# Kernel optimization log

Measured on AMD Instinct MI355X. Metric: run time of the kernel, lower is better.

## Reference

```python
import jax, jax.numpy as jnp
import numpy as np

P_FACTOR = 3.0
EPS = 1e-12  # torch F.normalize eps


def _l2norm(x):
    # F.normalize(x, dim=1): divide by max(||x||_2, eps) along feature dim
    n = jnp.sqrt(jnp.sum(x * x, axis=1, keepdims=True))
    return x / jnp.maximum(n, EPS)


def setup_inputs() -> dict:
    key = jax.random.key(0)
    ks = jax.random.split(key, 7)
    B, N, F, E = 4096, 20000, 768, 512
    X = jax.random.normal(ks[0], (B, F), jnp.float32)
    D = jax.random.normal(ks[1], (N, F), jnp.float32)
    r = jax.random.uniform(ks[2], (N, 1), jnp.float32)  # correctness in [0,1]
    g_w = jax.random.normal(ks[3], (E, F), jnp.float32) * (1.0 / np.sqrt(F))
    g_b = jax.random.normal(ks[4], (E,), jnp.float32) * 0.01
    h_w = jax.random.normal(ks[5], (1, 1), jnp.float32)
    h_b = jax.random.normal(ks[6], (1,), jnp.float32) * 0.01
    return {"X": X, "D": D, "r": r, "g_w": g_w, "g_b": g_b, "h_w": h_w, "h_b": h_b}


def reference(X, D, r, g_w, g_b, h_w, h_b):
    # register_buffer path: r = ex_correct * 2 - 1
    r = r * 2.0 - 1.0
    # g: Linear(feat_dim -> feat_embed_dim) on both queries and exemplars
    Xe = X @ g_w.T + g_b            # [B, E]
    De = D @ g_w.T + g_b            # [N, E]
    # h: Linear(1 -> class_embed_dim)
    rh = r @ h_w.T + h_b            # [N, C]
    # Minerva: cosine similarity -> power-law activation -> weighted retrieval
    a = _l2norm(Xe) @ _l2norm(De).T                 # [B, N]
    a = jnp.sign(a) * jnp.abs(a) ** P_FACTOR        # |s|^p * sign(s)
    logits = a @ rh                                 # [B, C]
    preds = jax.nn.sigmoid(logits)
    return logits, preds
```

## Files before the change

kernel.cpp:

```cpp
#include <hip/hip_runtime.h>
#include <cstdint>


typedef __attribute__((ext_vector_type(4))) float  f32x4;
typedef __attribute__((ext_vector_type(8))) __bf16 bf16x8;
typedef __attribute__((ext_vector_type(4))) __bf16 bf16x4;

constexpr int B = 4096, N = 20000, F = 768, E = 512;

#define AS1CAST(p) ((__attribute__((address_space(1))) unsigned int*)(uintptr_t)(p))
#define AS3CAST(p) ((__attribute__((address_space(3))) unsigned int*)(uintptr_t)(p))

__device__ __forceinline__ void gload_lds16(const void* g, void* l) {
  __builtin_amdgcn_global_load_lds(AS1CAST(g), AS3CAST(l), 16, 0, 0);
}


__global__ void k_prep(const float* __restrict__ X, const float* __restrict__ D,
                       const float* __restrict__ G, const float* __restrict__ r,
                       const float* __restrict__ hw, const float* __restrict__ hb,
                       __bf16* __restrict__ Xb, __bf16* __restrict__ Db,
                       __bf16* __restrict__ Gb, float* __restrict__ rh,
                       float* __restrict__ lg, float* __restrict__ norm2) {
  const int t = blockIdx.x * blockDim.x + threadIdx.x;
  const int stride = gridDim.x * blockDim.x;
  constexpr int nX = B * F / 4, nD = N * F / 4, nG = E * F / 4;
  constexpr int tot = nX + nD + nG;
  for (int i = t; i < tot; i += stride) {
    const float4* src; bf16x4* dst; int off;
    if (i < nX)           { src = (const float4*)X; dst = (bf16x4*)Xb; off = i; }
    else if (i < nX + nD) { src = (const float4*)D; dst = (bf16x4*)Db; off = i - nX; }
    else                  { src = (const float4*)G; dst = (bf16x4*)Gb; off = i - nX - nD; }
    float4 v = src[off];
    bf16x4 o;
    o[0] = (__bf16)v.x; o[1] = (__bf16)v.y; o[2] = (__bf16)v.z; o[3] = (__bf16)v.w;
    dst[off] = o;
  }
  if (t < N) rh[t] = (2.0f * r[t] - 1.0f) * hw[0] + hb[0];
  if (t < B) lg[t] = 0.0f;
  if (t < B + N) norm2[t] = 0.0f;
}


__global__ __launch_bounds__(256, 2)
void k_embed(const __bf16* __restrict__ Xb, const __bf16* __restrict__ Db,
             const __bf16* __restrict__ Gb, const float* __restrict__ bias,
             __bf16* __restrict__ Eb, float* __restrict__ norm2) {
  constexpr int K = F;
  __shared__ __bf16 As[128 * 32];
  __shared__ __bf16 Bs[128 * 32];
  __shared__ float ssum[128];
  const int tid  = threadIdx.x;
  const int wave = tid >> 6;
  const int lane = tid & 63;
  const int by = blockIdx.y;
  const bool isX = (by < B / 128);
  const __bf16* A = isX ? Xb : Db;
  const int m0 = isX ? by * 128 : (by - B / 128) * 128;
  const int Mr = isX ? B : N;
  const int g0 = by * 128;
  const int n0 = blockIdx.x * 128;
  if (tid < 128) ssum[tid] = 0.0f;

  const int r_in = lane >> 2;
  const int kp   = (lane & 3) * 8;
  int ar0 = m0 + wave * 16 + r_in;        if (ar0 >= Mr) ar0 = Mr - 1;
  int ar1 = m0 + (wave + 4) * 16 + r_in;  if (ar1 >= Mr) ar1 = Mr - 1;
  const int br0 = n0 + wave * 16 + r_in;
  const int br1 = n0 + (wave + 4) * 16 + r_in;

  const __bf16* ga0 = A + (size_t)ar0 * K + kp;
  const __bf16* ga1 = A + (size_t)ar1 * K + kp;
  const __bf16* gb0 = Gb + (size_t)br0 * K + kp;
  const __bf16* gb1 = Gb + (size_t)br1 * K + kp;
  __bf16* la0 = &As[(size_t)wave * 512 + (size_t)lane * 8];
  __bf16* la1 = &As[(size_t)(wave + 4) * 512 + (size_t)lane * 8];
  __bf16* lb0 = &Bs[(size_t)wave * 512 + (size_t)lane * 8];
  __bf16* lb1 = &Bs[(size_t)(wave + 4) * 512 + (size_t)lane * 8];

  const int mw = (wave & 1) * 64;
  const int nw = (wave >> 1) * 64;
  const int quad = lane >> 4;
  const int l15  = lane & 15;

  f32x4 acc[4][4] = {};

  for (int kb = 0; kb < K; kb += 32) {
    gload_lds16(ga0 + kb, la0);
    gload_lds16(ga1 + kb, la1);
    gload_lds16(gb0 + kb, lb0);
    gload_lds16(gb1 + kb, lb1);
    __syncthreads();
    bf16x8 af[4], bfr[4];
#pragma unroll
    for (int i = 0; i < 4; ++i)
      af[i] = *(const bf16x8*)&As[(mw + i * 16 + l15) * 32 + quad * 8];
#pragma unroll
    for (int j = 0; j < 4; ++j)
      bfr[j] = *(const bf16x8*)&Bs[(nw + j * 16 + l15) * 32 + quad * 8];
#pragma unroll
    for (int i = 0; i < 4; ++i)
#pragma unroll
      for (int j = 0; j < 4; ++j)
        acc[i][j] = __builtin_amdgcn_mfma_f32_16x16x32_bf16(af[i], bfr[j], acc[i][j], 0, 0, 0);
    __syncthreads();
  }

#pragma unroll
  for (int i = 0; i < 4; ++i) {
    float part[4] = {0.0f, 0.0f, 0.0f, 0.0f};
#pragma unroll
    for (int j = 0; j < 4; ++j) {
      const int col = n0 + nw + j * 16 + l15;
      const float bv = bias[col];
#pragma unroll
      for (int rr = 0; rr < 4; ++rr) {
        const int row = mw + i * 16 + quad * 4 + rr;
        if (m0 + row < Mr) {
          const __bf16 hv = (__bf16)(acc[i][j][rr] + bv);
          Eb[(size_t)(g0 + row) * E + col] = hv;
          const float vb = (float)hv;
          part[rr] += vb * vb;
        }
      }
    }
#pragma unroll
    for (int rr = 0; rr < 4; ++rr) {
      float v = part[rr];
      v += __shfl_xor(v, 1);
      v += __shfl_xor(v, 2);
      v += __shfl_xor(v, 4);
      v += __shfl_xor(v, 8);
      if (l15 == 0) atomicAdd(&ssum[mw + i * 16 + quad * 4 + rr], v);
    }
  }
  __syncthreads();
  if (tid < 128 && m0 + tid < Mr) atomicAdd(&norm2[g0 + tid], ssum[tid]);
}


__global__ void k_normall(const __bf16* __restrict__ Eb, const float* __restrict__ norm2,
                          __bf16* __restrict__ Nb, int rows) {
  const int row  = blockIdx.x * 4 + (threadIdx.x >> 6);
  const int lane = threadIdx.x & 63;
  if (row >= rows) return;
  bf16x8 v = ((const bf16x8*)(Eb + (size_t)row * E))[lane];
  const float sc = 1.0f / fmaxf(sqrtf(norm2[row]), 1e-12f);
  bf16x8 o;
#pragma unroll
  for (int k = 0; k < 8; ++k) o[k] = (__bf16)((float)v[k] * sc);
  ((bf16x8*)(Nb + (size_t)row * E))[lane] = o;
}


__global__ __launch_bounds__(256, 2)
void k_minerva(const __bf16* __restrict__ Xn, const __bf16* __restrict__ Dn,
               const float* __restrict__ rh, float* __restrict__ logits) {
  constexpr int K  = 512;
  constexpr int MT = B / 128;
  constexpr int NT = (N + 127) / 128;
  constexpr int W  = 20;
  __shared__ __bf16 As[128 * 64];
  __shared__ __bf16 Bs[128 * 64];
  __shared__ float lsum[128];
  const int tid  = threadIdx.x;
  const int lane = tid & 63;
  const int wave = tid >> 6;

  const int bid   = blockIdx.x;
  const int panel = bid / (W * MT);
  const int bn    = panel * W;
  const int Wp    = min(W, NT - bn);
  const int rem   = bid - panel * (W * MT);
  const int mt    = rem / Wp;
  const int nt    = bn + rem % Wp;
  const int m0 = mt * 128, n0 = nt * 128;
  if (tid < 128) lsum[tid] = 0.0f;

  const int srow = tid >> 3;
  const int scg  = (tid & 7) ^ (srow & 7);
  const __bf16* ga[4];
  const __bf16* gb[4];
  __bf16* la[4];
  __bf16* lb[4];
#pragma unroll
  for (int q = 0; q < 4; ++q) {
    const int row = srow + q * 32;
    const int arow = m0 + row;
    int brow = n0 + row; if (brow >= N) brow = N - 1;
    ga[q] = Xn + (size_t)arow * K + scg * 8;
    gb[q] = Dn + (size_t)brow * K + scg * 8;
    la[q] = &As[q * 2048 + tid * 8];
    lb[q] = &Bs[q * 2048 + tid * 8];
  }

  const int mw = (wave & 1) * 64;
  const int nw = (wave >> 1) * 64;
  const int quad = lane >> 4;
  const int l15  = lane & 15;
  f32x4 acc[4][4] = {};

  for (int kb = 0; kb < K; kb += 64) {
#pragma unroll
    for (int q = 0; q < 4; ++q) gload_lds16(ga[q] + kb, la[q]);
#pragma unroll
    for (int q = 0; q < 4; ++q) gload_lds16(gb[q] + kb, lb[q]);
    __syncthreads();
#pragma unroll
    for (int h = 0; h < 2; ++h) {
      bf16x8 af[4], bfr[4];
#pragma unroll
      for (int i = 0; i < 4; ++i) {
        const int r = mw + i * 16 + l15;
        af[i] = *(const bf16x8*)&As[r * 64 + ((quad + h * 4) ^ (r & 7)) * 8];
      }
#pragma unroll
      for (int j = 0; j < 4; ++j) {
        const int r = nw + j * 16 + l15;
        bfr[j] = *(const bf16x8*)&Bs[r * 64 + ((quad + h * 4) ^ (r & 7)) * 8];
      }
#pragma unroll
      for (int i = 0; i < 4; ++i)
#pragma unroll
        for (int j = 0; j < 4; ++j)
          acc[i][j] = __builtin_amdgcn_mfma_f32_16x16x32_bf16(af[i], bfr[j], acc[i][j], 0, 0, 0);
    }
    __syncthreads();
  }

  float rhv[4];
#pragma unroll
  for (int j = 0; j < 4; ++j) {
    const int col = n0 + nw + j * 16 + l15;
    rhv[j] = (col < N) ? rh[col] : 0.0f;
  }
#pragma unroll
  for (int i = 0; i < 4; ++i) {
    float part[4] = {0.0f, 0.0f, 0.0f, 0.0f};
#pragma unroll
    for (int j = 0; j < 4; ++j)
#pragma unroll
      for (int rr = 0; rr < 4; ++rr) {
        const float s = acc[i][j][rr];
        part[rr] += s * s * s * rhv[j];
      }
#pragma unroll
    for (int rr = 0; rr < 4; ++rr) {
      float v = part[rr];
      v += __shfl_xor(v, 1);
      v += __shfl_xor(v, 2);
      v += __shfl_xor(v, 4);
      v += __shfl_xor(v, 8);
      if (l15 == 0) atomicAdd(&lsum[mw + i * 16 + quad * 4 + rr], v);
    }
  }
  __syncthreads();
  if (tid < 128) atomicAdd(&logits[m0 + tid], lsum[tid]);
}


__global__ void k_finalize(const float* __restrict__ logits, float* __restrict__ out, int n) {
  int i = blockIdx.x * blockDim.x + threadIdx.x;
  if (i < n) {
    float L = logits[i];
    out[i] = L;
    out[n + i] = 1.0f / (1.0f + expf(-L));
  }
}


extern "C" void kernel_launch(void* const* d_in, const int* in_sizes, int n_in,
                              void* d_out, int out_size, void* d_ws, size_t ws_size,
                              hipStream_t stream) {
  const float* X   = (const float*)d_in[0];
  const float* D   = (const float*)d_in[1];
  const float* r   = (const float*)d_in[2];
  const float* g_w = (const float*)d_in[3];
  const float* g_b = (const float*)d_in[4];
  const float* h_w = (const float*)d_in[5];
  const float* h_b = (const float*)d_in[6];
  float* out = (float*)d_out;

  char* ws = (char*)d_ws;
  __bf16* Xb    = (__bf16*)(ws + 0);
  __bf16* Db    = (__bf16*)(ws + 6291456);
  __bf16* Gb    = (__bf16*)(ws + 37011456);
  __bf16* Eb    = (__bf16*)(ws + 37797888);
  __bf16* Nb    = (__bf16*)(ws + 62472192);
  float*  rh    = (float*) (ws + 87146496);
  float*  norm2 = (float*) (ws + 87226496);
  float*  lg    = (float*) (ws + 87322880);

  k_prep<<<2048, 256, 0, stream>>>(X, D, g_w, r, h_w, h_b, Xb, Db, Gb, rh, lg, norm2);

  k_embed<<<dim3(E / 128, B / 128 + (N + 127) / 128), 256, 0, stream>>>(
      Xb, Db, Gb, g_b, Eb, norm2);

  k_normall<<<(B + N + 3) / 4, 256, 0, stream>>>(Eb, norm2, Nb, B + N);

  k_minerva<<<7 * 20 * 32 + 17 * 32, 256, 0, stream>>>(Nb, Nb + (size_t)B * E, rh, lg);

  k_finalize<<<(B + 255) / 256, 256, 0, stream>>>(lg, out, B);
}
```

Before: 258.7 us.

## Fold L2 normalization into minerva epilogue, widen embed K-tile with swizzled LDS

Removes the separate normalization kernel and its write of a normalized bf16 copy. The minerva GEMM now reads the unnormalized embeddings and applies the inverse norms cubed in its epilogue, using the identity (a/(|x||d|))^3 = a^3/|x|^3/|d|^3. The embed GEMM moves to a 64-wide K tile with XOR-swizzled LDS loads, matching the minerva kernel. Both GEMMs request 3 blocks per SM, and minerva's block-to-tile mapping now walks M tiles first within each N panel. The risks are larger dot products before scaling, which slightly changes bf16 rounding, and register pressure from the tighter launch bound.

```diff
diff --git a/kernel.cpp b/kernel.cpp
--- a/kernel.cpp
+++ b/kernel.cpp
@@ -42,13 +42,13 @@
 }
 
 
-__global__ __launch_bounds__(256, 2)
+__global__ __launch_bounds__(256, 3)
 void k_embed(const __bf16* __restrict__ Xb, const __bf16* __restrict__ Db,
              const __bf16* __restrict__ Gb, const float* __restrict__ bias,
              __bf16* __restrict__ Eb, float* __restrict__ norm2) {
   constexpr int K = F;
-  __shared__ __bf16 As[128 * 32];
-  __shared__ __bf16 Bs[128 * 32];
+  __shared__ __bf16 As[128 * 64];
+  __shared__ __bf16 Bs[128 * 64];
   __shared__ float ssum[128];
   const int tid  = threadIdx.x;
   const int wave = tid >> 6;
@@ -62,47 +62,54 @@
   const int n0 = blockIdx.x * 128;
   if (tid < 128) ssum[tid] = 0.0f;
 
-  const int r_in = lane >> 2;
-  const int kp   = (lane & 3) * 8;
-  int ar0 = m0 + wave * 16 + r_in;        if (ar0 >= Mr) ar0 = Mr - 1;
-  int ar1 = m0 + (wave + 4) * 16 + r_in;  if (ar1 >= Mr) ar1 = Mr - 1;
-  const int br0 = n0 + wave * 16 + r_in;
-  const int br1 = n0 + (wave + 4) * 16 + r_in;
-
-  const __bf16* ga0 = A + (size_t)ar0 * K + kp;
-  const __bf16* ga1 = A + (size_t)ar1 * K + kp;
-  const __bf16* gb0 = Gb + (size_t)br0 * K + kp;
-  const __bf16* gb1 = Gb + (size_t)br1 * K + kp;
-  __bf16* la0 = &As[(size_t)wave * 512 + (size_t)lane * 8];
-  __bf16* la1 = &As[(size_t)(wave + 4) * 512 + (size_t)lane * 8];
-  __bf16* lb0 = &Bs[(size_t)wave * 512 + (size_t)lane * 8];
-  __bf16* lb1 = &Bs[(size_t)(wave + 4) * 512 + (size_t)lane * 8];
+  const int srow = tid >> 3;
+  const int scg  = (tid & 7) ^ (srow & 7);
+  const __bf16* ga[4];
+  const __bf16* gb[4];
+  __bf16* la[4];
+  __bf16* lb[4];
+#pragma unroll
+  for (int q = 0; q < 4; ++q) {
+    const int row = srow + q * 32;
+    int arow = m0 + row; if (arow >= Mr) arow = Mr - 1;
+    const int brow = n0 + row;
+    ga[q] = A  + (size_t)arow * K + scg * 8;
+    gb[q] = Gb + (size_t)brow * K + scg * 8;
+    la[q] = &As[q * 2048 + tid * 8];
+    lb[q] = &Bs[q * 2048 + tid * 8];
+  }
 
   const int mw = (wave & 1) * 64;
   const int nw = (wave >> 1) * 64;
   const int quad = lane >> 4;
   const int l15  = lane & 15;
-
   f32x4 acc[4][4] = {};
 
-  for (int kb = 0; kb < K; kb += 32) {
-    gload_lds16(ga0 + kb, la0);
-    gload_lds16(ga1 + kb, la1);
-    gload_lds16(gb0 + kb, lb0);
-    gload_lds16(gb1 + kb, lb1);
+  for (int kb = 0; kb < K; kb += 64) {
+#pragma unroll
+    for (int q = 0; q < 4; ++q) gload_lds16(ga[q] + kb, la[q]);
+#pragma unroll
+    for (int q = 0; q < 4; ++q) gload_lds16(gb[q] + kb, lb[q]);
     __syncthreads();
-    bf16x8 af[4], bfr[4];
-#pragma unroll
-    for (int i = 0; i < 4; ++i)
-      af[i] = *(const bf16x8*)&As[(mw + i * 16 + l15) * 32 + quad * 8];
-#pragma unroll
-    for (int j = 0; j < 4; ++j)
-      bfr[j] = *(const bf16x8*)&Bs[(nw + j * 16 + l15) * 32 + quad * 8];
-#pragma unroll
-    for (int i = 0; i < 4; ++i)
-#pragma unroll
-      for (int j = 0; j < 4; ++j)
-        acc[i][j] = __builtin_amdgcn_mfma_f32_16x16x32_bf16(af[i], bfr[j], acc[i][j], 0, 0, 0);
+#pragma unroll
+    for (int h = 0; h < 2; ++h) {
+      bf16x8 af[4], bfr[4];
+#pragma unroll
+      for (int i = 0; i < 4; ++i) {
+        const int rr = mw + i * 16 + l15;
+        af[i] = *(const bf16x8*)&As[rr * 64 + ((quad + h * 4) ^ (rr & 7)) * 8];
+      }
+#pragma unroll
+      for (int j = 0; j < 4; ++j) {
+        const int rr = nw + j * 16 + l15;
+        bfr[j] = *(const bf16x8*)&Bs[rr * 64 + ((quad + h * 4) ^ (rr & 7)) * 8];
+      }
+#pragma unroll
+      for (int i = 0; i < 4; ++i)
+#pragma unroll
+        for (int j = 0; j < 4; ++j)
+          acc[i][j] = __builtin_amdgcn_mfma_f32_16x16x32_bf16(af[i], bfr[j], acc[i][j], 0, 0, 0);
+    }
     __syncthreads();
   }
 
@@ -139,23 +146,10 @@
 }
 
 
-__global__ void k_normall(const __bf16* __restrict__ Eb, const float* __restrict__ norm2,
-                          __bf16* __restrict__ Nb, int rows) {
-  const int row  = blockIdx.x * 4 + (threadIdx.x >> 6);
-  const int lane = threadIdx.x & 63;
-  if (row >= rows) return;
-  bf16x8 v = ((const bf16x8*)(Eb + (size_t)row * E))[lane];
-  const float sc = 1.0f / fmaxf(sqrtf(norm2[row]), 1e-12f);
-  bf16x8 o;
-#pragma unroll
-  for (int k = 0; k < 8; ++k) o[k] = (__bf16)((float)v[k] * sc);
-  ((bf16x8*)(Nb + (size_t)row * E))[lane] = o;
-}
-
-
-__global__ __launch_bounds__(256, 2)
-void k_minerva(const __bf16* __restrict__ Xn, const __bf16* __restrict__ Dn,
-               const float* __restrict__ rh, float* __restrict__ logits) {
+__global__ __launch_bounds__(256, 3)
+void k_minerva(const __bf16* __restrict__ Xe, const __bf16* __restrict__ De,
+               const float* __restrict__ norm2, const float* __restrict__ rh,
+               float* __restrict__ logits) {
   constexpr int K  = 512;
   constexpr int MT = B / 128;
   constexpr int NT = (N + 127) / 128;
@@ -170,10 +164,9 @@
   const int bid   = blockIdx.x;
   const int panel = bid / (W * MT);
   const int bn    = panel * W;
-  const int Wp    = min(W, NT - bn);
   const int rem   = bid - panel * (W * MT);
-  const int mt    = rem / Wp;
-  const int nt    = bn + rem % Wp;
+  const int mt    = rem % MT;
+  const int nt    = bn + rem / MT;
   const int m0 = mt * 128, n0 = nt * 128;
   if (tid < 128) lsum[tid] = 0.0f;
 
@@ -188,8 +181,8 @@
     const int row = srow + q * 32;
     const int arow = m0 + row;
     int brow = n0 + row; if (brow >= N) brow = N - 1;
-    ga[q] = Xn + (size_t)arow * K + scg * 8;
-    gb[q] = Dn + (size_t)brow * K + scg * 8;
+    ga[q] = Xe + (size_t)arow * K + scg * 8;
+    gb[q] = De + (size_t)brow * K + scg * 8;
     la[q] = &As[q * 2048 + tid * 8];
     lb[q] = &Bs[q * 2048 + tid * 8];
   }
@@ -211,13 +204,13 @@
       bf16x8 af[4], bfr[4];
 #pragma unroll
       for (int i = 0; i < 4; ++i) {
-        const int r = mw + i * 16 + l15;
-        af[i] = *(const bf16x8*)&As[r * 64 + ((quad + h * 4) ^ (r & 7)) * 8];
+        const int rr = mw + i * 16 + l15;
+        af[i] = *(const bf16x8*)&As[rr * 64 + ((quad + h * 4) ^ (rr & 7)) * 8];
       }
 #pragma unroll
       for (int j = 0; j < 4; ++j) {
-        const int r = nw + j * 16 + l15;
-        bfr[j] = *(const bf16x8*)&Bs[r * 64 + ((quad + h * 4) ^ (r & 7)) * 8];
+        const int rr = nw + j * 16 + l15;
+        bfr[j] = *(const bf16x8*)&Bs[rr * 64 + ((quad + h * 4) ^ (rr & 7)) * 8];
       }
 #pragma unroll
       for (int i = 0; i < 4; ++i)
@@ -228,25 +221,36 @@
     __syncthreads();
   }
 
-  float rhv[4];
+  float id3rh[4];
 #pragma unroll
   for (int j = 0; j < 4; ++j) {
     const int col = n0 + nw + j * 16 + l15;
-    rhv[j] = (col < N) ? rh[col] : 0.0f;
+    if (col < N) {
+      const float id = 1.0f / fmaxf(sqrtf(norm2[B + col]), 1e-12f);
+      id3rh[j] = id * id * id * rh[col];
+    } else id3rh[j] = 0.0f;
   }
 #pragma unroll
   for (int i = 0; i < 4; ++i) {
+    float ix3[4];
+#pragma unroll
+    for (int rr = 0; rr < 4; ++rr) {
+      const int row = m0 + mw + i * 16 + quad * 4 + rr;
+      const float ix = 1.0f / fmaxf(sqrtf(norm2[row]), 1e-12f);
+      ix3[rr] = ix * ix * ix;
+    }
     float part[4] = {0.0f, 0.0f, 0.0f, 0.0f};
 #pragma unroll
     for (int j = 0; j < 4; ++j)
 #pragma unroll
       for (int rr = 0; rr < 4; ++rr) {
-        const float s = acc[i][j][rr];
-        part[rr] += s * s * s * rhv[j];
+        const float a = acc[i][j][rr];
+        const float a2 = a * a;
+        part[rr] = fmaf(a2 * a, id3rh[j], part[rr]);
       }
 #pragma unroll
     for (int rr = 0; rr < 4; ++rr) {
-      float v = part[rr];
+      float v = part[rr] * ix3[rr];
       v += __shfl_xor(v, 1);
       v += __shfl_xor(v, 2);
       v += __shfl_xor(v, 4);
@@ -286,19 +290,16 @@
   __bf16* Db    = (__bf16*)(ws + 6291456);
   __bf16* Gb    = (__bf16*)(ws + 37011456);
   __bf16* Eb    = (__bf16*)(ws + 37797888);
-  __bf16* Nb    = (__bf16*)(ws + 62472192);
-  float*  rh    = (float*) (ws + 87146496);
-  float*  norm2 = (float*) (ws + 87226496);
-  float*  lg    = (float*) (ws + 87322880);
+  float*  rh    = (float*) (ws + 62472192);
+  float*  norm2 = (float*) (ws + 62552192);
+  float*  lg    = (float*) (ws + 62648576);
 
   k_prep<<<2048, 256, 0, stream>>>(X, D, g_w, r, h_w, h_b, Xb, Db, Gb, rh, lg, norm2);
 
   k_embed<<<dim3(E / 128, B / 128 + (N + 127) / 128), 256, 0, stream>>>(
       Xb, Db, Gb, g_b, Eb, norm2);
 
-  k_normall<<<(B + N + 3) / 4, 256, 0, stream>>>(Eb, norm2, Nb, B + N);
-
-  k_minerva<<<7 * 20 * 32 + 17 * 32, 256, 0, stream>>>(Nb, Nb + (size_t)B * E, rh, lg);
+  k_minerva<<<157 * 32, 256, 0, stream>>>(Eb, Eb + (size_t)B * E, norm2, rh, lg);
 
   k_finalize<<<(B + 255) / 256, 256, 0, stream>>>(lg, out, B);
 }
```

After: 257.5 us. Within noise of the previous version (-0.5%).
